# Kernel tuning notes

Hardware: AMD Instinct MI355X
Metric: run time of the kernel (lower is better)

Reference implementation:

```python
import jax, jax.numpy as jnp
import numpy as np

V = 32000   # vocab_size
T = 2048    # train_len (pos embed table size)
E = 1024    # embed_dim
H = 16      # num_heads
FF = 4096   # ff_dim
L = 4       # num_layers
B, C = 2, 1024
D = E // H  # head_dim = 64
EPS = 1e-5


def setup_inputs() -> dict:
    key = jax.random.key(0)
    ks = jax.random.split(key, 12)
    s = 0.02
    inp = {
        "x": jax.random.randint(ks[0], (B, C), 0, V),
        "embed": jax.random.normal(ks[1], (V, E), jnp.float32) * s,
        "pos_embed": jax.random.normal(ks[2], (T, E), jnp.float32) * s,
        "Wq": jax.random.normal(ks[3], (L, E, E), jnp.float32) * s,
        "Wk": jax.random.normal(ks[4], (L, E, E), jnp.float32) * s,
        "Wv": jax.random.normal(ks[5], (L, E, E), jnp.float32) * s,
        "Wo": jax.random.normal(ks[6], (L, E, E), jnp.float32) * s,
        "ln1_w": jnp.ones((L, E), jnp.float32),
        "ln1_b": jnp.zeros((L, E), jnp.float32),
        "ln2_w": jnp.ones((L, E), jnp.float32),
        "ln2_b": jnp.zeros((L, E), jnp.float32),
        "W1": jax.random.normal(ks[7], (L, E, FF), jnp.float32) * s,
        "b1": jnp.zeros((L, FF), jnp.float32),
        "W2": jax.random.normal(ks[8], (L, FF, E), jnp.float32) * s,
        "b2": jnp.zeros((L, E), jnp.float32),
        "lnf_w": jnp.ones((E,), jnp.float32),
        "lnf_b": jnp.zeros((E,), jnp.float32),
        "Wout": jax.random.normal(ks[9], (E, V), jnp.float32) * s,
        "bout": jnp.zeros((V,), jnp.float32),
    }
    return inp


def _layernorm(h, w, b):
    mu = jnp.mean(h, axis=-1, keepdims=True)
    var = jnp.var(h, axis=-1, keepdims=True)
    return (h - mu) * jax.lax.rsqrt(var + EPS) * w + b


def reference(x, embed, pos_embed, Wq, Wk, Wv, Wo, ln1_w, ln1_b, ln2_w, ln2_b,
              W1, b1, W2, b2, lnf_w, lnf_b, Wout, bout):
    Bx, Cx = x.shape
    positions = jnp.clip(jnp.arange(Cx), 0, T - 1)  # 'clamp' extrapolation
    h = embed[x] + pos_embed[positions]             # [B,C,E]
    # causal mask: -inf above the diagonal
    mask = jnp.where(jnp.tril(jnp.ones((Cx, Cx), bool)), 0.0, -jnp.inf).astype(h.dtype)
    scale = 1.0 / np.sqrt(D)
    for i in range(L):
        hn = _layernorm(h, ln1_w[i], ln1_b[i])
        Q = (hn @ Wq[i]).reshape(Bx, Cx, H, D).transpose(0, 2, 1, 3)  # [B,H,C,D]
        K = (hn @ Wk[i]).reshape(Bx, Cx, H, D).transpose(0, 2, 1, 3)
        Vv = (hn @ Wv[i]).reshape(Bx, Cx, H, D).transpose(0, 2, 1, 3)
        scores = jnp.einsum('bhqd,bhkd->bhqk', Q, K) * scale + mask
        weights = jax.nn.softmax(scores, axis=-1)
        attn = jnp.einsum('bhqk,bhkd->bhqd', weights, Vv)
        attn = attn.transpose(0, 2, 1, 3).reshape(Bx, Cx, E) @ Wo[i]
        h = h + attn
        hn2 = _layernorm(h, ln2_w[i], ln2_b[i])
        h = h + jax.nn.gelu(hn2 @ W1[i] + b1[i], approximate=False) @ W2[i] + b2[i]
    return _layernorm(h, lnf_w, lnf_b) @ Wout + bout  # [B,C,V]
```

## Files before the change

### kernel.cpp

```cpp
#include <hip/hip_runtime.h>
#include <hip/hip_bf16.h>
#include <math.h>

constexpr int V  = 32000;
constexpr int E  = 1024;
constexpr int H  = 16;
constexpr int FF = 4096;
constexpr int L  = 4;
constexpr int B  = 2;
constexpr int C  = 1024;
constexpr int D  = 64;
constexpr int N  = B * C;
constexpr int E3 = 3 * E;
constexpr float EPS = 1e-5f;

typedef __hip_bfloat16 bf16;
typedef __bf16 bf16x8 __attribute__((ext_vector_type(8)));
typedef __bf16 bf16x4 __attribute__((ext_vector_type(4)));
typedef float  f32x4  __attribute__((ext_vector_type(4)));

#define AS1 __attribute__((address_space(1)))
#define AS3 __attribute__((address_space(3)))

__device__ inline bf16x8 lds_load8(const bf16* p) {
    bf16x4 lo = *(const bf16x4*)p;
    bf16x4 hi = *(const bf16x4*)(p + 4);
    bf16x8 r;
    r[0]=lo[0]; r[1]=lo[1]; r[2]=lo[2]; r[3]=lo[3];
    r[4]=hi[0]; r[5]=hi[1]; r[6]=hi[2]; r[7]=hi[3];
    return r;
}
__device__ inline void lds_store8(bf16* p, bf16x8 v) {
    bf16x4 lo, hi;
    lo[0]=v[0]; lo[1]=v[1]; lo[2]=v[2]; lo[3]=v[3];
    hi[0]=v[4]; hi[1]=v[5]; hi[2]=v[6]; hi[3]=v[7];
    *(bf16x4*)p = lo; *(bf16x4*)(p + 4) = hi;
}

__device__ inline bf16x8 lds_frag(const bf16* sbase, int row, int chunk) {
    return *(const bf16x8*)(sbase + (row >> 3) * 512 + (row & 7) * 64 +
                            ((chunk ^ (row & 7)) << 3));
}

__global__ void embed_kernel(const int* __restrict__ x,
                             const float* __restrict__ embed,
                             const float* __restrict__ pos,
                             float* __restrict__ h) {
    int token = blockIdx.x;
    int c = token % C;
    int id = x[token];
    const float* erow = embed + (size_t)id * E;
    const float* prow = pos   + (size_t)c  * E;
    float* hrow = h + (size_t)token * E;
    for (int e = threadIdx.x; e < E; e += blockDim.x)
        hrow[e] = erow[e] + prow[e];
}

__global__ void layernorm_kernel(const float* __restrict__ in,
                                 const float* __restrict__ w,
                                 const float* __restrict__ b,
                                 bf16* __restrict__ out) {
    __shared__ float red[256];
    int token = blockIdx.x;
    int tid = threadIdx.x;
    float4 xv = ((const float4*)(in + (size_t)token * E))[tid];

    red[tid] = xv.x + xv.y + xv.z + xv.w;
    __syncthreads();
    for (int st = 128; st > 0; st >>= 1) {
        if (tid < st) red[tid] += red[tid + st];
        __syncthreads();
    }
    float mu = red[0] * (1.0f / E);
    __syncthreads();

    float d0 = xv.x - mu, d1 = xv.y - mu, d2 = xv.z - mu, d3 = xv.w - mu;
    red[tid] = d0 * d0 + d1 * d1 + d2 * d2 + d3 * d3;
    __syncthreads();
    for (int st = 128; st > 0; st >>= 1) {
        if (tid < st) red[tid] += red[tid + st];
        __syncthreads();
    }
    float var = red[0] * (1.0f / E);
    float inv = rsqrtf(var + EPS);

    float4 wv = ((const float4*)w)[tid];
    float4 bv = ((const float4*)b)[tid];
    float y0 = d0 * inv * wv.x + bv.x;
    float y1 = d1 * inv * wv.y + bv.y;
    float y2 = d2 * inv * wv.z + bv.z;
    float y3 = d3 * inv * wv.w + bv.w;
    ushort4 o;
    { bf16 t0 = __float2bfloat16(y0); o.x = *(ushort*)&t0; }
    { bf16 t1 = __float2bfloat16(y1); o.y = *(ushort*)&t1; }
    { bf16 t2 = __float2bfloat16(y2); o.z = *(ushort*)&t2; }
    { bf16 t3 = __float2bfloat16(y3); o.w = *(ushort*)&t3; }
    ((ushort4*)(out + (size_t)token * E))[tid] = o;
}

__global__ void transpose_bf16(const float* __restrict__ in,
                               bf16* __restrict__ out, int K, int Nn) {
    __shared__ float tile[32][33];
    int n0 = blockIdx.x * 32, k0 = blockIdx.y * 32;
    int tx = threadIdx.x & 31, ty = threadIdx.x >> 5;
    #pragma unroll
    for (int i = 0; i < 32; i += 8)
        tile[ty + i][tx] = in[(size_t)(k0 + ty + i) * Nn + n0 + tx];
    __syncthreads();
    #pragma unroll
    for (int i = 0; i < 32; i += 8)
        out[(size_t)(n0 + ty + i) * K + k0 + tx] = __float2bfloat16(tile[tx][ty + i]);
}

__global__ void transpose_v(const bf16* __restrict__ qkv,
                            bf16* __restrict__ vt) {
    __shared__ ushort tile[32][34];
    int c0 = blockIdx.x * 32;
    int d0 = (blockIdx.y & 1) * 32;
    int bh = blockIdx.y >> 1;
    int bb = bh >> 4, hh = bh & 15;
    int tx = threadIdx.x & 31, ty = threadIdx.x >> 5;
    const ushort* src = (const ushort*)qkv;
    ushort* dst = (ushort*)vt;
    #pragma unroll
    for (int i = 0; i < 32; i += 8)
        tile[ty + i][tx] = src[(size_t)(bb * C + c0 + ty + i) * E3 + 2 * E + hh * D + d0 + tx];
    __syncthreads();
    #pragma unroll
    for (int i = 0; i < 32; i += 8)
        dst[((size_t)bh * D + d0 + ty + i) * C + c0 + tx] = tile[tx][ty + i];
}

__launch_bounds__(256, 2)
__global__ void gemm_bf16_128(const bf16* __restrict__ A,
                              const bf16* __restrict__ Bt,
                              const float* __restrict__ bias,
                              const float* __restrict__ res,
                              float* __restrict__ outF,
                              bf16*  __restrict__ outB,
                              int M, int Nc, int K, int gelu_flag) {
    __shared__ __align__(16) bf16 sA[2][128 * 64];
    __shared__ __align__(16) bf16 sB[2][128 * 64];

    int tid  = threadIdx.x;
    int lane = tid & 63;
    int wid  = tid >> 6;
    int wr   = wid >> 1;
    int wc   = wid & 1;
    int l16  = lane & 15;
    int lhi  = lane >> 4;

    int nwg = gridDim.x * gridDim.y;
    int id  = blockIdx.y * gridDim.x + blockIdx.x;
    int cpx = nwg >> 3;
    int swz = (id & 7) * cpx + (id >> 3);
    int bx  = swz % gridDim.x;
    int by  = swz / gridDim.x;

    size_t brow = (size_t)by * 128;
    size_t bcol = (size_t)bx * 128;

    f32x4 acc[4][4] = {};

    auto stage = [&](int buf, int t) {
        size_t k0 = (size_t)t * 64;
        #pragma unroll
        for (int s = 0; s < 4; ++s) {
            int slot = s * 256 + tid;
            int row  = slot >> 3;
            int ch   = (slot & 7) ^ (row & 7);
            int ldso = (s * 256 + wid * 64) * 8;
            const bf16* ga = A + (brow + row) * K + k0 + ch * 8;
            __builtin_amdgcn_global_load_lds(
                (const AS1 void*)ga, (AS3 void*)(&sA[buf][0] + ldso), 16, 0, 0);
        }
        #pragma unroll
        for (int s = 0; s < 4; ++s) {
            int slot = s * 256 + tid;
            int row  = slot >> 3;
            int ch   = (slot & 7) ^ (row & 7);
            int ldso = (s * 256 + wid * 64) * 8;
            const bf16* gb = Bt + (bcol + row) * K + k0 + ch * 8;
            __builtin_amdgcn_global_load_lds(
                (const AS1 void*)gb, (AS3 void*)(&sB[buf][0] + ldso), 16, 0, 0);
        }
    };

    int NT = K / 64;
    stage(0, 0);

    for (int t = 0; t < NT; ++t) {
        if (t + 1 < NT) {
            stage((t + 1) & 1, t + 1);
            asm volatile("s_waitcnt vmcnt(8)" ::: "memory");
        } else {
            asm volatile("s_waitcnt vmcnt(0)" ::: "memory");
        }
        __builtin_amdgcn_sched_barrier(0);
        __builtin_amdgcn_s_barrier();

        const bf16* As_ = &sA[t & 1][0];
        const bf16* Bs_ = &sB[t & 1][0];
        bf16x8 ra[4][2], rb[4][2];
        #pragma unroll
        for (int m = 0; m < 4; ++m)
            #pragma unroll
            for (int kh = 0; kh < 2; ++kh)
                ra[m][kh] = lds_frag(As_, wr * 64 + m * 16 + l16, kh * 4 + lhi);
        #pragma unroll
        for (int n = 0; n < 4; ++n)
            #pragma unroll
            for (int kh = 0; kh < 2; ++kh)
                rb[n][kh] = lds_frag(Bs_, wc * 64 + n * 16 + l16, kh * 4 + lhi);

        __builtin_amdgcn_s_setprio(1);
        #pragma unroll
        for (int m = 0; m < 4; ++m)
            #pragma unroll
            for (int n = 0; n < 4; ++n)
                #pragma unroll
                for (int kh = 0; kh < 2; ++kh)
                    acc[m][n] = __builtin_amdgcn_mfma_f32_16x16x32_bf16(
                        ra[m][kh], rb[n][kh], acc[m][n], 0, 0, 0);
        __builtin_amdgcn_s_setprio(0);
        __builtin_amdgcn_s_barrier();
    }

    int crow = lhi * 4;
    #pragma unroll
    for (int m = 0; m < 4; ++m) {
        #pragma unroll
        for (int n = 0; n < 4; ++n) {
            #pragma unroll
            for (int r = 0; r < 4; ++r) {
                size_t row = brow + wr * 64 + m * 16 + crow + r;
                size_t col = bcol + wc * 64 + n * 16 + l16;
                float val = acc[m][n][r];
                if (bias) val += bias[col];
                if (gelu_flag) val = 0.5f * val * (1.0f + erff(val * 0.70710678118f));
                if (res) val += res[row * Nc + col];
                if (outF) outF[row * Nc + col] = val;
                if (outB) outB[row * Nc + col] = __float2bfloat16(val);
            }
        }
    }
}

constexpr int TBM = 256, TBN = 256, TBK = 64;

__launch_bounds__(512, 2)
__global__ void gemm_bf16_256(const bf16* __restrict__ A,
                              const bf16* __restrict__ Bt,
                              const float* __restrict__ bias,
                              const float* __restrict__ res,
                              float* __restrict__ outF,
                              bf16*  __restrict__ outB,
                              int M, int Nc, int K, int gelu_flag) {
    __shared__ __align__(16) bf16 sA[2][TBM * TBK];
    __shared__ __align__(16) bf16 sB[2][TBN * TBK];

    int tid  = threadIdx.x;
    int lane = tid & 63;
    int wid  = tid >> 6;
    int wm   = wid >> 2;
    int wn   = wid & 3;
    int l16  = lane & 15;
    int lhi  = lane >> 4;

    int nwg = gridDim.x * gridDim.y;
    int id  = blockIdx.y * gridDim.x + blockIdx.x;
    int cpx = nwg >> 3;
    int swz = (id & 7) * cpx + (id >> 3);
    int bx  = swz % gridDim.x;
    int by  = swz / gridDim.x;

    size_t brow = (size_t)by * TBM;
    size_t bcol = (size_t)bx * TBN;

    f32x4 acc[8][4] = {};

    auto stage = [&](int buf, int t) {
        size_t k0 = (size_t)t * TBK;
        #pragma unroll
        for (int it = 0; it < 4; ++it) {
            int s  = it * 512 + tid;
            int li = s & 63;
            int row = (s >> 6) * 8 + (li >> 3);
            int c8  = (li & 7) ^ (li >> 3);
            int ldsbase = (it * 512 + wid * 64) * 8;
            const bf16* ga = A  + (brow + row) * K + k0 + c8 * 8;
            const bf16* gb = Bt + (bcol + row) * K + k0 + c8 * 8;
            __builtin_amdgcn_global_load_lds(
                (const AS1 void*)ga, (AS3 void*)(sA[buf] + ldsbase), 16, 0, 0);
            __builtin_amdgcn_global_load_lds(
                (const AS1 void*)gb, (AS3 void*)(sB[buf] + ldsbase), 16, 0, 0);
        }
    };

    int NT = K / TBK;
    stage(0, 0);

    for (int t = 0; t < NT; ++t) {
        if (t + 1 < NT) {
            stage((t + 1) & 1, t + 1);
            asm volatile("s_waitcnt vmcnt(8)" ::: "memory");
        } else {
            asm volatile("s_waitcnt vmcnt(0)" ::: "memory");
        }
        __builtin_amdgcn_sched_barrier(0);
        __builtin_amdgcn_s_barrier();

        const bf16* As_ = sA[t & 1];
        const bf16* Bs_ = sB[t & 1];
        bf16x8 ra[4][2], rb[2][2];

        #pragma unroll
        for (int m = 0; m < 4; ++m)
            #pragma unroll
            for (int kh = 0; kh < 2; ++kh)
                ra[m][kh] = lds_frag(As_, wm * 128 + m * 16 + l16, kh * 4 + lhi);
        #pragma unroll
        for (int n = 0; n < 2; ++n)
            #pragma unroll
            for (int kh = 0; kh < 2; ++kh)
                rb[n][kh] = lds_frag(Bs_, wn * 64 + n * 16 + l16, kh * 4 + lhi);
        __builtin_amdgcn_s_setprio(1);
        #pragma unroll
        for (int m = 0; m < 4; ++m)
            #pragma unroll
            for (int n = 0; n < 2; ++n)
                #pragma unroll
                for (int kh = 0; kh < 2; ++kh)
                    acc[m][n] = __builtin_amdgcn_mfma_f32_16x16x32_bf16(
                        ra[m][kh], rb[n][kh], acc[m][n], 0, 0, 0);
        __builtin_amdgcn_s_setprio(0);

        #pragma unroll
        for (int n = 0; n < 2; ++n)
            #pragma unroll
            for (int kh = 0; kh < 2; ++kh)
                rb[n][kh] = lds_frag(Bs_, wn * 64 + (n + 2) * 16 + l16, kh * 4 + lhi);
        __builtin_amdgcn_s_setprio(1);
        #pragma unroll
        for (int m = 0; m < 4; ++m)
            #pragma unroll
            for (int n = 0; n < 2; ++n)
                #pragma unroll
                for (int kh = 0; kh < 2; ++kh)
                    acc[m][n + 2] = __builtin_amdgcn_mfma_f32_16x16x32_bf16(
                        ra[m][kh], rb[n][kh], acc[m][n + 2], 0, 0, 0);
        __builtin_amdgcn_s_setprio(0);

        #pragma unroll
        for (int m = 0; m < 4; ++m)
            #pragma unroll
            for (int kh = 0; kh < 2; ++kh)
                ra[m][kh] = lds_frag(As_, wm * 128 + (m + 4) * 16 + l16, kh * 4 + lhi);
        __builtin_amdgcn_s_setprio(1);
        #pragma unroll
        for (int m = 0; m < 4; ++m)
            #pragma unroll
            for (int n = 0; n < 2; ++n)
                #pragma unroll
                for (int kh = 0; kh < 2; ++kh)
                    acc[m + 4][n + 2] = __builtin_amdgcn_mfma_f32_16x16x32_bf16(
                        ra[m][kh], rb[n][kh], acc[m + 4][n + 2], 0, 0, 0);
        __builtin_amdgcn_s_setprio(0);

        #pragma unroll
        for (int n = 0; n < 2; ++n)
            #pragma unroll
            for (int kh = 0; kh < 2; ++kh)
                rb[n][kh] = lds_frag(Bs_, wn * 64 + n * 16 + l16, kh * 4 + lhi);
        __builtin_amdgcn_s_setprio(1);
        #pragma unroll
        for (int m = 0; m < 4; ++m)
            #pragma unroll
            for (int n = 0; n < 2; ++n)
                #pragma unroll
                for (int kh = 0; kh < 2; ++kh)
                    acc[m + 4][n] = __builtin_amdgcn_mfma_f32_16x16x32_bf16(
                        ra[m][kh], rb[n][kh], acc[m + 4][n], 0, 0, 0);
        __builtin_amdgcn_s_setprio(0);

        __builtin_amdgcn_s_barrier();
    }

    int crow = lhi * 4;
    #pragma unroll
    for (int m = 0; m < 8; ++m) {
        #pragma unroll
        for (int n = 0; n < 4; ++n) {
            #pragma unroll
            for (int r = 0; r < 4; ++r) {
                size_t row = brow + wm * 128 + m * 16 + crow + r;
                size_t col = bcol + wn * 64 + n * 16 + l16;
                float val = acc[m][n][r];
                if (bias) val += bias[col];
                if (gelu_flag) val = 0.5f * val * (1.0f + erff(val * 0.70710678118f));
                if (res) val += res[row * Nc + col];
                if (outF) __builtin_nontemporal_store(val, &outF[row * Nc + col]);
                if (outB) outB[row * Nc + col] = __float2bfloat16(val);
            }
        }
    }
}

constexpr int QBLK = 64;
constexpr int KVB  = 64;
constexpr int PSTR = 72;

__launch_bounds__(256)
__global__ void flash_attn(const bf16* __restrict__ qkv,
                           const bf16* __restrict__ vt,
                           bf16* __restrict__ O) {
    __shared__ bf16 sK[KVB][PSTR];
    __shared__ bf16 sV[D][PSTR];
    __shared__ bf16 sP[4][16][PSTR];

    int qt = blockIdx.x;
    int bh = blockIdx.y;
    int bb = bh >> 4, hh = bh & 15;
    int qbase = qt * QBLK;
    int tid = threadIdx.x, lane = tid & 63, w = tid >> 6;
    int l16 = lane & 15, lhi = lane >> 4;

    int qrow = qbase + w * 16 + l16;
    const bf16* qp = qkv + (size_t)(bb * C + qrow) * E3 + hh * D + lhi * 8;
    bf16x8 qf0 = *(const bf16x8*)qp;
    bf16x8 qf1 = *(const bf16x8*)(qp + 32);

    f32x4 oa[4] = {};
    float m_run[4] = {-INFINITY, -INFINITY, -INFINITY, -INFINITY};
    float l_run[4] = {0.f, 0.f, 0.f, 0.f};

    for (int t = 0; t <= qt; ++t) {
        int k0 = t * KVB;
        #pragma unroll
        for (int it = 0; it < 2; ++it) {
            int s = it * 256 + tid;
            int row = s >> 3, c8 = s & 7;
            bf16x8 kv = *(const bf16x8*)(qkv + (size_t)(bb * C + k0 + row) * E3 + E + hh * D + c8 * 8);
            lds_store8(&sK[row][c8 * 8], kv);
            bf16x8 vv = *(const bf16x8*)(vt + ((size_t)bh * D + row) * C + k0 + c8 * 8);
            lds_store8(&sV[row][c8 * 8], vv);
        }
        __syncthreads();

        f32x4 sc[4] = {};
        #pragma unroll
        for (int n = 0; n < 4; ++n) {
            bf16x8 kf0 = lds_load8(&sK[n * 16 + l16][lhi * 8]);
            sc[n] = __builtin_amdgcn_mfma_f32_16x16x32_bf16(qf0, kf0, sc[n], 0, 0, 0);
            bf16x8 kf1 = lds_load8(&sK[n * 16 + l16][32 + lhi * 8]);
            sc[n] = __builtin_amdgcn_mfma_f32_16x16x32_bf16(qf1, kf1, sc[n], 0, 0, 0);
        }

        int qg = qbase + w * 16 + lhi * 4;
        #pragma unroll
        for (int n = 0; n < 4; ++n) {
            int kg = k0 + n * 16 + l16;
            #pragma unroll
            for (int r = 0; r < 4; ++r) {
                float vvv = sc[n][r] * 0.125f;
                if (t == qt && kg > qg + r) vvv = -1e30f;
                sc[n][r] = vvv;
            }
        }

        float pm[4];
        #pragma unroll
        for (int r = 0; r < 4; ++r)
            pm[r] = fmaxf(fmaxf(sc[0][r], sc[1][r]), fmaxf(sc[2][r], sc[3][r]));
        #pragma unroll
        for (int xm = 1; xm <= 8; xm <<= 1)
            #pragma unroll
            for (int r = 0; r < 4; ++r)
                pm[r] = fmaxf(pm[r], __shfl_xor(pm[r], xm));

        float corr[4];
        #pragma unroll
        for (int r = 0; r < 4; ++r) {
            float mn = fmaxf(m_run[r], pm[r]);
            corr[r] = __expf(m_run[r] - mn);
            m_run[r] = mn;
        }
        f32x4 p[4];
        #pragma unroll
        for (int n = 0; n < 4; ++n)
            #pragma unroll
            for (int r = 0; r < 4; ++r)
                p[n][r] = __expf(sc[n][r] - m_run[r]);

        float rsum[4];
        #pragma unroll
        for (int r = 0; r < 4; ++r)
            rsum[r] = p[0][r] + p[1][r] + p[2][r] + p[3][r];
        #pragma unroll
        for (int xm = 1; xm <= 8; xm <<= 1)
            #pragma unroll
            for (int r = 0; r < 4; ++r)
                rsum[r] += __shfl_xor(rsum[r], xm);
        #pragma unroll
        for (int r = 0; r < 4; ++r)
            l_run[r] = l_run[r] * corr[r] + rsum[r];
        #pragma unroll
        for (int nd = 0; nd < 4; ++nd)
            #pragma unroll
            for (int r = 0; r < 4; ++r)
                oa[nd][r] *= corr[r];

        #pragma unroll
        for (int n = 0; n < 4; ++n)
            #pragma unroll
            for (int r = 0; r < 4; ++r)
                sP[w][lhi * 4 + r][n * 16 + l16] = __float2bfloat16(p[n][r]);
        bf16x8 pa0 = lds_load8(&sP[w][l16][lhi * 8]);
        bf16x8 pa1 = lds_load8(&sP[w][l16][32 + lhi * 8]);

        #pragma unroll
        for (int nd = 0; nd < 4; ++nd) {
            bf16x8 vf0 = lds_load8(&sV[nd * 16 + l16][lhi * 8]);
            oa[nd] = __builtin_amdgcn_mfma_f32_16x16x32_bf16(pa0, vf0, oa[nd], 0, 0, 0);
            bf16x8 vf1 = lds_load8(&sV[nd * 16 + l16][32 + lhi * 8]);
            oa[nd] = __builtin_amdgcn_mfma_f32_16x16x32_bf16(pa1, vf1, oa[nd], 0, 0, 0);
        }
        __syncthreads();
    }

    #pragma unroll
    for (int r = 0; r < 4; ++r) {
        float inv = 1.0f / l_run[r];
        int qg = qbase + w * 16 + lhi * 4 + r;
        bf16* orow = O + (size_t)(bb * C + qg) * E + hh * D;
        #pragma unroll
        for (int nd = 0; nd < 4; ++nd)
            orow[nd * 16 + l16] = __float2bfloat16(oa[nd][r] * inv);
    }
}

extern "C" void kernel_launch(void* const* d_in, const int* in_sizes, int n_in,
                              void* d_out, int out_size, void* d_ws, size_t ws_size,
                              hipStream_t stream) {
    const int*   x     = (const int*)  d_in[0];
    const float* embed = (const float*)d_in[1];
    const float* pos   = (const float*)d_in[2];
    const float* Wq    = (const float*)d_in[3];
    const float* Wk    = (const float*)d_in[4];
    const float* Wv    = (const float*)d_in[5];
    const float* Wo    = (const float*)d_in[6];
    const float* ln1w  = (const float*)d_in[7];
    const float* ln1b  = (const float*)d_in[8];
    const float* ln2w  = (const float*)d_in[9];
    const float* ln2b  = (const float*)d_in[10];
    const float* W1    = (const float*)d_in[11];
    const float* b1    = (const float*)d_in[12];
    const float* W2    = (const float*)d_in[13];
    const float* b2    = (const float*)d_in[14];
    const float* lnfw  = (const float*)d_in[15];
    const float* lnfb  = (const float*)d_in[16];
    const float* Wout  = (const float*)d_in[17];
    const float* bout  = (const float*)d_in[18];
    float* out = (float*)d_out;

    char* p = (char*)d_ws;
    auto alloc = [&](size_t bytes) {
        char* r = p;
        p += (bytes + 255) & ~(size_t)255;
        return r;
    };
    float* h    = (float*)alloc((size_t)N * E  * 4);
    bf16*  qkvb = (bf16*) alloc((size_t)N * E3 * 2);
    bf16*  hn   = (bf16*) alloc((size_t)N * E  * 2);
    bf16*  attn = (bf16*) alloc((size_t)N * E  * 2);
    bf16*  ff   = (bf16*) alloc((size_t)N * FF * 2);
    bf16*  vt   = (bf16*) alloc((size_t)B * H * D * C * 2);
    bf16*  qkvt = (bf16*) alloc((size_t)L * E3 * E * 2);
    bf16*  wot  = (bf16*) alloc((size_t)L * E  * E * 2);
    bf16*  w1t  = (bf16*) alloc((size_t)L * FF * E * 2);
    bf16*  w2t  = (bf16*) alloc((size_t)L * E  * FF * 2);
    bf16*  wvt  = (bf16*) alloc((size_t)V * E  * 2);

    for (int i = 0; i < L; ++i) {
        transpose_bf16<<<dim3(E / 32, E / 32), 256, 0, stream>>>(
            Wq + (size_t)i * E * E, qkvt + ((size_t)i * E3 + 0 * E) * E, E, E);
        transpose_bf16<<<dim3(E / 32, E / 32), 256, 0, stream>>>(
            Wk + (size_t)i * E * E, qkvt + ((size_t)i * E3 + 1 * E) * E, E, E);
        transpose_bf16<<<dim3(E / 32, E / 32), 256, 0, stream>>>(
            Wv + (size_t)i * E * E, qkvt + ((size_t)i * E3 + 2 * E) * E, E, E);
        transpose_bf16<<<dim3(E / 32, E / 32), 256, 0, stream>>>(
            Wo + (size_t)i * E * E, wot + (size_t)i * E * E, E, E);
        transpose_bf16<<<dim3(FF / 32, E / 32), 256, 0, stream>>>(
            W1 + (size_t)i * E * FF, w1t + (size_t)i * FF * E, E, FF);
        transpose_bf16<<<dim3(E / 32, FF / 32), 256, 0, stream>>>(
            W2 + (size_t)i * FF * E, w2t + (size_t)i * E * FF, FF, E);
    }
    transpose_bf16<<<dim3(V / 32, E / 32), 256, 0, stream>>>(Wout, wvt, E, V);

    embed_kernel<<<N, 256, 0, stream>>>(x, embed, pos, h);

    dim3 gQKV(E3 / 128, N / 128);
    dim3 gE  (E  / 128, N / 128);
    dim3 gF  (FF / 128, N / 128);
    dim3 gV  (V  / TBN, N / TBM);

    for (int i = 0; i < L; ++i) {
        layernorm_kernel<<<N, 256, 0, stream>>>(h, ln1w + i * E, ln1b + i * E, hn);

        gemm_bf16_128<<<gQKV, 256, 0, stream>>>(hn, qkvt + (size_t)i * E3 * E,
                                                nullptr, nullptr, nullptr, qkvb,
                                                N, E3, E, 0);

        transpose_v<<<dim3(C / 32, 2 * B * H), 256, 0, stream>>>(qkvb, vt);

        flash_attn<<<dim3(C / QBLK, B * H), 256, 0, stream>>>(qkvb, vt, attn);

        gemm_bf16_128<<<gE, 256, 0, stream>>>(attn, wot + (size_t)i * E * E,
                                              nullptr, h, h, nullptr,
                                              N, E, E, 0);

        layernorm_kernel<<<N, 256, 0, stream>>>(h, ln2w + i * E, ln2b + i * E, hn);

        gemm_bf16_128<<<gF, 256, 0, stream>>>(hn, w1t + (size_t)i * FF * E,
                                              b1 + (size_t)i * FF, nullptr,
                                              nullptr, ff,
                                              N, FF, E, 1);
        gemm_bf16_128<<<gE, 256, 0, stream>>>(ff, w2t + (size_t)i * E * FF,
                                              b2 + (size_t)i * E, h, h, nullptr,
                                              N, E, FF, 0);
    }

    layernorm_kernel<<<N, 256, 0, stream>>>(h, lnfw, lnfb, hn);
    gemm_bf16_256<<<gV, 512, 0, stream>>>(hn, wvt, bout, nullptr, out, nullptr,
                                          N, V, E, 0);
}
```

Before: 1.483 ms.

## Use 64x128 tiles for N=1024 GEMMs, drop 256 tile for vocab projection

Replaces the 256x256 GEMM kernel with a 64x128 tile kernel used for the Wo and W2 projections (output width 1024), doubling the workgroup count to better fill the GPU's compute units. The vocab projection now uses the existing 128x128 kernel, which also drops the nontemporal store for its large output. The block swizzle is changed to map consecutive ids down columns (row-major over gridDim.y) in both kernels. Smaller tiles reduce per-block reuse and raise global traffic, and the 128 kernel on the vocab GEMM may be less efficient than the 256 one.

```diff
diff --git a/kernel.cpp b/kernel.cpp
--- a/kernel.cpp
+++ b/kernel.cpp
@@ -154,8 +154,8 @@
     int id  = blockIdx.y * gridDim.x + blockIdx.x;
     int cpx = nwg >> 3;
     int swz = (id & 7) * cpx + (id >> 3);
-    int bx  = swz % gridDim.x;
-    int by  = swz / gridDim.x;
+    int bx  = swz / gridDim.y;
+    int by  = swz % gridDim.y;
 
     size_t brow = (size_t)by * 128;
     size_t bcol = (size_t)bx * 128;
@@ -246,24 +246,20 @@
     }
 }
 
-constexpr int TBM = 256, TBN = 256, TBK = 64;
-
-__launch_bounds__(512, 2)
-__global__ void gemm_bf16_256(const bf16* __restrict__ A,
-                              const bf16* __restrict__ Bt,
-                              const float* __restrict__ bias,
-                              const float* __restrict__ res,
-                              float* __restrict__ outF,
-                              bf16*  __restrict__ outB,
-                              int M, int Nc, int K, int gelu_flag) {
-    __shared__ __align__(16) bf16 sA[2][TBM * TBK];
-    __shared__ __align__(16) bf16 sB[2][TBN * TBK];
+__launch_bounds__(256, 3)
+__global__ void gemm_bf16_64(const bf16* __restrict__ A,
+                             const bf16* __restrict__ Bt,
+                             const float* __restrict__ bias,
+                             const float* __restrict__ res,
+                             float* __restrict__ outF,
+                             bf16*  __restrict__ outB,
+                             int M, int Nc, int K, int gelu_flag) {
+    __shared__ __align__(16) bf16 sA[2][64 * 64];
+    __shared__ __align__(16) bf16 sB[2][128 * 64];
 
     int tid  = threadIdx.x;
     int lane = tid & 63;
     int wid  = tid >> 6;
-    int wm   = wid >> 2;
-    int wn   = wid & 3;
     int l16  = lane & 15;
     int lhi  = lane >> 4;
 
@@ -271,59 +267,65 @@
     int id  = blockIdx.y * gridDim.x + blockIdx.x;
     int cpx = nwg >> 3;
     int swz = (id & 7) * cpx + (id >> 3);
-    int bx  = swz % gridDim.x;
-    int by  = swz / gridDim.x;
-
-    size_t brow = (size_t)by * TBM;
-    size_t bcol = (size_t)bx * TBN;
-
-    f32x4 acc[8][4] = {};
+    int bx  = swz / gridDim.y;
+    int by  = swz % gridDim.y;
+
+    size_t brow = (size_t)by * 64;
+    size_t bcol = (size_t)bx * 128;
+
+    f32x4 acc[4][2] = {};
 
     auto stage = [&](int buf, int t) {
-        size_t k0 = (size_t)t * TBK;
-        #pragma unroll
-        for (int it = 0; it < 4; ++it) {
-            int s  = it * 512 + tid;
-            int li = s & 63;
-            int row = (s >> 6) * 8 + (li >> 3);
-            int c8  = (li & 7) ^ (li >> 3);
-            int ldsbase = (it * 512 + wid * 64) * 8;
-            const bf16* ga = A  + (brow + row) * K + k0 + c8 * 8;
-            const bf16* gb = Bt + (bcol + row) * K + k0 + c8 * 8;
+        size_t k0 = (size_t)t * 64;
+        #pragma unroll
+        for (int s = 0; s < 2; ++s) {
+            int slot = s * 256 + tid;
+            int row  = slot >> 3;
+            int ch   = (slot & 7) ^ (row & 7);
+            int ldso = (s * 256 + wid * 64) * 8;
+            const bf16* ga = A + (brow + row) * K + k0 + ch * 8;
             __builtin_amdgcn_global_load_lds(
-                (const AS1 void*)ga, (AS3 void*)(sA[buf] + ldsbase), 16, 0, 0);
+                (const AS1 void*)ga, (AS3 void*)(&sA[buf][0] + ldso), 16, 0, 0);
+        }
+        #pragma unroll
+        for (int s = 0; s < 4; ++s) {
+            int slot = s * 256 + tid;
+            int row  = slot >> 3;
+            int ch   = (slot & 7) ^ (row & 7);
+            int ldso = (s * 256 + wid * 64) * 8;
+            const bf16* gb = Bt + (bcol + row) * K + k0 + ch * 8;
             __builtin_amdgcn_global_load_lds(
-                (const AS1 void*)gb, (AS3 void*)(sB[buf] + ldsbase), 16, 0, 0);
+                (const AS1 void*)gb, (AS3 void*)(&sB[buf][0] + ldso), 16, 0, 0);
         }
     };
 
-    int NT = K / TBK;
+    int NT = K / 64;
     stage(0, 0);
 
     for (int t = 0; t < NT; ++t) {
         if (t + 1 < NT) {
             stage((t + 1) & 1, t + 1);
-            asm volatile("s_waitcnt vmcnt(8)" ::: "memory");
+            asm volatile("s_waitcnt vmcnt(6)" ::: "memory");
         } else {
             asm volatile("s_waitcnt vmcnt(0)" ::: "memory");
         }
         __builtin_amdgcn_sched_barrier(0);
         __builtin_amdgcn_s_barrier();
 
-        const bf16* As_ = sA[t & 1];
-        const bf16* Bs_ = sB[t & 1];
+        const bf16* As_ = &sA[t & 1][0];
+        const bf16* Bs_ = &sB[t & 1][0];
         bf16x8 ra[4][2], rb[2][2];
-
         #pragma unroll
         for (int m = 0; m < 4; ++m)
             #pragma unroll
             for (int kh = 0; kh < 2; ++kh)
-                ra[m][kh] = lds_frag(As_, wm * 128 + m * 16 + l16, kh * 4 + lhi);
+                ra[m][kh] = lds_frag(As_, m * 16 + l16, kh * 4 + lhi);
         #pragma unroll
         for (int n = 0; n < 2; ++n)
             #pragma unroll
             for (int kh = 0; kh < 2; ++kh)
-                rb[n][kh] = lds_frag(Bs_, wn * 64 + n * 16 + l16, kh * 4 + lhi);
+                rb[n][kh] = lds_frag(Bs_, wid * 32 + n * 16 + l16, kh * 4 + lhi);
+
         __builtin_amdgcn_s_setprio(1);
         #pragma unroll
         for (int m = 0; m < 4; ++m)
@@ -334,72 +336,23 @@
                     acc[m][n] = __builtin_amdgcn_mfma_f32_16x16x32_bf16(
                         ra[m][kh], rb[n][kh], acc[m][n], 0, 0, 0);
         __builtin_amdgcn_s_setprio(0);
-
-        #pragma unroll
-        for (int n = 0; n < 2; ++n)
-            #pragma unroll
-            for (int kh = 0; kh < 2; ++kh)
-                rb[n][kh] = lds_frag(Bs_, wn * 64 + (n + 2) * 16 + l16, kh * 4 + lhi);
-        __builtin_amdgcn_s_setprio(1);
-        #pragma unroll
-        for (int m = 0; m < 4; ++m)
-            #pragma unroll
-            for (int n = 0; n < 2; ++n)
-                #pragma unroll
-                for (int kh = 0; kh < 2; ++kh)
-                    acc[m][n + 2] = __builtin_amdgcn_mfma_f32_16x16x32_bf16(
-                        ra[m][kh], rb[n][kh], acc[m][n + 2], 0, 0, 0);
-        __builtin_amdgcn_s_setprio(0);
-
-        #pragma unroll
-        for (int m = 0; m < 4; ++m)
-            #pragma unroll
-            for (int kh = 0; kh < 2; ++kh)
-                ra[m][kh] = lds_frag(As_, wm * 128 + (m + 4) * 16 + l16, kh * 4 + lhi);
-        __builtin_amdgcn_s_setprio(1);
-        #pragma unroll
-        for (int m = 0; m < 4; ++m)
-            #pragma unroll
-            for (int n = 0; n < 2; ++n)
-                #pragma unroll
-                for (int kh = 0; kh < 2; ++kh)
-                    acc[m + 4][n + 2] = __builtin_amdgcn_mfma_f32_16x16x32_bf16(
-                        ra[m][kh], rb[n][kh], acc[m + 4][n + 2], 0, 0, 0);
-        __builtin_amdgcn_s_setprio(0);
-
-        #pragma unroll
-        for (int n = 0; n < 2; ++n)
-            #pragma unroll
-            for (int kh = 0; kh < 2; ++kh)
-                rb[n][kh] = lds_frag(Bs_, wn * 64 + n * 16 + l16, kh * 4 + lhi);
-        __builtin_amdgcn_s_setprio(1);
-        #pragma unroll
-        for (int m = 0; m < 4; ++m)
-            #pragma unroll
-            for (int n = 0; n < 2; ++n)
-                #pragma unroll
-                for (int kh = 0; kh < 2; ++kh)
-                    acc[m + 4][n] = __builtin_amdgcn_mfma_f32_16x16x32_bf16(
-                        ra[m][kh], rb[n][kh], acc[m + 4][n], 0, 0, 0);
-        __builtin_amdgcn_s_setprio(0);
-
         __builtin_amdgcn_s_barrier();
     }
 
     int crow = lhi * 4;
     #pragma unroll
-    for (int m = 0; m < 8; ++m) {
-        #pragma unroll
-        for (int n = 0; n < 4; ++n) {
+    for (int m = 0; m < 4; ++m) {
+        #pragma unroll
+        for (int n = 0; n < 2; ++n) {
             #pragma unroll
             for (int r = 0; r < 4; ++r) {
-                size_t row = brow + wm * 128 + m * 16 + crow + r;
-                size_t col = bcol + wn * 64 + n * 16 + l16;
+                size_t row = brow + m * 16 + crow + r;
+                size_t col = bcol + wid * 32 + n * 16 + l16;
                 float val = acc[m][n][r];
                 if (bias) val += bias[col];
                 if (gelu_flag) val = 0.5f * val * (1.0f + erff(val * 0.70710678118f));
                 if (res) val += res[row * Nc + col];
-                if (outF) __builtin_nontemporal_store(val, &outF[row * Nc + col]);
+                if (outF) outF[row * Nc + col] = val;
                 if (outB) outB[row * Nc + col] = __float2bfloat16(val);
             }
         }
@@ -600,9 +553,9 @@
     embed_kernel<<<N, 256, 0, stream>>>(x, embed, pos, h);
 
     dim3 gQKV(E3 / 128, N / 128);
-    dim3 gE  (E  / 128, N / 128);
     dim3 gF  (FF / 128, N / 128);
-    dim3 gV  (V  / TBN, N / TBM);
+    dim3 gV  (V  / 128, N / 128);
+    dim3 gO  (E  / 128, N / 64);
 
     for (int i = 0; i < L; ++i) {
         layernorm_kernel<<<N, 256, 0, stream>>>(h, ln1w + i * E, ln1b + i * E, hn);
@@ -615,9 +568,9 @@
 
         flash_attn<<<dim3(C / QBLK, B * H), 256, 0, stream>>>(qkvb, vt, attn);
 
-        gemm_bf16_128<<<gE, 256, 0, stream>>>(attn, wot + (size_t)i * E * E,
-                                              nullptr, h, h, nullptr,
-                                              N, E, E, 0);
+        gemm_bf16_64<<<gO, 256, 0, stream>>>(attn, wot + (size_t)i * E * E,
+                                             nullptr, h, h, nullptr,
+                                             N, E, E, 0);
 
         layernorm_kernel<<<N, 256, 0, stream>>>(h, ln2w + i * E, ln2b + i * E, hn);
 
@@ -625,12 +578,12 @@
                                               b1 + (size_t)i * FF, nullptr,
                                               nullptr, ff,
                                               N, FF, E, 1);
-        gemm_bf16_128<<<gE, 256, 0, stream>>>(ff, w2t + (size_t)i * E * FF,
-                                              b2 + (size_t)i * E, h, h, nullptr,
-                                              N, E, FF, 0);
+        gemm_bf16_64<<<gO, 256, 0, stream>>>(ff, w2t + (size_t)i * E * FF,
+                                             b2 + (size_t)i * E, h, h, nullptr,
+                                             N, E, FF, 0);
     }
 
     layernorm_kernel<<<N, 256, 0, stream>>>(h, lnfw, lnfb, hn);
-    gemm_bf16_256<<<gV, 512, 0, stream>>>(hn, wvt, bout, nullptr, out, nullptr,
+    gemm_bf16_128<<<gV, 256, 0, stream>>>(hn, wvt, bout, nullptr, out, nullptr,
                                           N, V, E, 0);
 }
```

Result: faster. 1.382 ms (-6.8%).
